# Performance work log

Measured on AMD Instinct MI355X. Metric: run time of the kernel, lower is better.

## Reference

```python
import jax, jax.numpy as jnp
import numpy as np

S, L, T, E, H = 88, 10, 30, 768, 64  # stocks, lookback days, texts/day, embed, hidden


def setup_inputs() -> dict:
    ks = iter(jax.random.split(jax.random.key(0), 40))

    def p(shape, s=0.05):
        return (jax.random.normal(next(ks), shape) * s).astype(jnp.float32)

    inp = {
        'text_inputs': jax.random.normal(next(ks), (S, L, T, E), jnp.float32),
        'time_inputs': jax.random.uniform(next(ks), (S, L, T), jnp.float32),
        # per-stock TimeLSTM params (torch Linear stored as [in,out])
        'Wd_w': p((S, H, H)), 'Wd_b': p((S, H)),
        'Wall_w': p((S, H, 4 * H)), 'Wall_b': p((S, 4 * H)),
        'Uall_w': p((S, E, 4 * H)), 'Uall_b': p((S, 4 * H)),
        # per-stock text attention
        'tW1_w': p((S, H, H)), 'tW1_b': p((S, H)),
        'tW2_w': p((S, H, H)), 'tW2_b': p((S, H)),
        'tV_w': p((S, H, 1)), 'tV_b': p((S, 1)),
        # per-stock day nn.LSTM cell (h0=0 so W_hh contributes nothing; keep its bias)
        'ih_w': p((S, H, 4 * H)), 'ih_b': p((S, 4 * H)), 'hh_b': p((S, 4 * H)),
        # per-stock day attention
        'dW1_w': p((S, H, H)), 'dW1_b': p((S, H)),
        'dW2_w': p((S, H, H)), 'dW2_b': p((S, H)),
        'dV_w': p((S, H, 1)), 'dV_b': p((S, 1)),
        # shared prediction head
        'pred_w': p((H, 1)), 'pred_b': p((1,)),
    }
    return inp


def _fast_forward(text_inputs, time_inputs, Wd_w, Wd_b, Wall_w, Wall_b, Uall_w, Uall_b,
                  tW1_w, tW1_b, tW2_w, tW2_b, tV_w, tV_b,
                  ih_w, ih_b, hh_b, dW1_w, dW1_b, dW2_w, dW2_b, dV_w, dV_b,
                  pred_w, pred_b):
    # Precompute input projection U_all(x): [S,L,T,4H]
    u = jnp.einsum('slte,seg->sltg', text_inputs, Uall_w) + Uall_b[:, None, None, :]

    def step(carry, xs):
        h, c = carry                      # each [S,L,H]
        u_t, ts_t = xs                    # [S,L,4H], [S,L]
        c_s1 = jnp.tanh(jnp.einsum('slh,shk->slk', c, Wd_w) + Wd_b[:, None, :])
        c_adj = c - c_s1 + c_s1 * ts_t[..., None]
        gates = jnp.einsum('slh,shg->slg', h, Wall_w) + Wall_b[:, None, :] + u_t
        f, i, o, g = jnp.split(jax.nn.sigmoid(gates), 4, axis=-1)  # all sigmoid (incl. candidate, as in source)
        c = f * c_adj + i * g
        h = o * jnp.tanh(c)
        return (h, c), h

    z = jnp.zeros((S, L, H), text_inputs.dtype)
    (h_last, _), hs = jax.lax.scan(step, (z, z), (jnp.moveaxis(u, 2, 0), jnp.moveaxis(time_inputs, 2, 0)))
    full = jnp.moveaxis(hs, 0, 2)  # [S,L,T,H]

    # text attention: softmax over texts T
    a1 = jnp.einsum('slh,shk->slk', h_last, tW1_w) + tW1_b[:, None, :]
    a2 = jnp.einsum('slth,shk->sltk', full, tW2_w) + tW2_b[:, None, None, :]
    score = jnp.einsum('slth,sho->slto', jnp.tanh(a1[:, :, None, :] + a2), tV_w) + tV_b[:, None, None, :]
    attn = jax.nn.softmax(score, axis=2)
    day_vec = jnp.sum(attn * full, axis=2)  # [S,L,H]

    # day nn.LSTM: input (1,L,64) seq-first => seq_len=1, batch=L -> single step from zero state
    gates = jnp.einsum('slh,shg->slg', day_vec, ih_w) + ih_b[:, None, :] + hh_b[:, None, :]
    i_g, f_g, g_g, o_g = jnp.split(gates, 4, axis=-1)  # torch gate order i,f,g,o
    c_d = jax.nn.sigmoid(i_g) * jnp.tanh(g_g)
    h_d = jax.nn.sigmoid(o_g) * jnp.tanh(c_d)  # [S,L,H]; output == h_n since seq_len==1

    # day attention: full == last == h_d, softmax over days L
    b1 = jnp.einsum('slh,shk->slk', h_d, dW1_w) + dW1_b[:, None, :]
    b2 = jnp.einsum('slh,shk->slk', h_d, dW2_w) + dW2_b[:, None, :]
    score_d = jnp.einsum('slh,sho->slo', jnp.tanh(b1 + b2), dV_w) + dV_b[:, None, :]
    attn_d = jax.nn.softmax(score_d, axis=1)
    stock_vec = jnp.sum(attn_d * h_d, axis=1)  # [S,H]

    return jax.nn.leaky_relu(stock_vec @ pred_w + pred_b)  # [S,1], slope 0.01


def reference(text_inputs, time_inputs, Wd_w, Wd_b, Wall_w, Wall_b, Uall_w, Uall_b,
              tW1_w, tW1_b, tW2_w, tW2_b, tV_w, tV_b,
              ih_w, ih_b, hh_b, dW1_w, dW1_b, dW2_w, dW2_b, dV_w, dV_b,
              pred_w, pred_b):
    return _fast_forward(text_inputs, time_inputs, Wd_w, Wd_b, Wall_w, Wall_b, Uall_w, Uall_b,
                         tW1_w, tW1_b, tW2_w, tW2_b, tV_w, tV_b,
                         ih_w, ih_b, hh_b, dW1_w, dW1_b, dW2_w, dW2_b, dV_w, dV_b,
                         pred_w, pred_b)
```

## Files before the change

kernel.cpp:

```cpp
#include <hip/hip_runtime.h>
#include <cmath>

#define NS 88
#define NL 10
#define NT 30
#define NE 768
#define NH 64
#define NG 256
#define NM 300

typedef _Float16 half_t;
typedef __attribute__((ext_vector_type(2))) _Float16 half2_t;
typedef __attribute__((ext_vector_type(8))) _Float16 half8;
typedef __attribute__((ext_vector_type(4))) _Float16 half4v;
typedef __attribute__((ext_vector_type(4))) float f32x4;

__device__ inline void gload_lds16(const void* g, void* l) {
  __builtin_amdgcn_global_load_lds(
      (const __attribute__((address_space(1))) unsigned int*)g,
      (__attribute__((address_space(3))) unsigned int*)l, 16, 0, 0);
}

__device__ inline float fsigmoid(float x) {
  return __builtin_amdgcn_rcpf(1.f + __expf(-x));
}
__device__ inline float ftanh(float x) {
  float e = __expf(2.f * x);
  return 1.f - 2.f * __builtin_amdgcn_rcpf(e + 1.f);
}

#if __has_builtin(__builtin_amdgcn_fdot2)
__device__ inline float fdot2(half2_t a, half2_t b, float c) {
  return __builtin_amdgcn_fdot2(a, b, c, false);
}
#else
__device__ inline float fdot2(half2_t a, half2_t b, float c) {
  return fmaf((float)a[1], (float)b[1], fmaf((float)a[0], (float)b[0], c));
}
#endif

__device__ inline half2_t mk_h2(float a, float b) {
  half2_t r; r[0] = (half_t)a; r[1] = (half_t)b; return r;
}

__global__ __launch_bounds__(256) void convB_kernel(
    const float* __restrict__ in, half_t* __restrict__ out)
{
  __shared__ float tile[32][36];
  int b  = blockIdx.x;
  int s  = b / 192;
  int r  = b % 192;
  int kt = r / 8;
  int nt = r % 8;
  int t  = threadIdx.x;

  int kk  = t >> 3;
  int nn4 = (t & 7) * 4;
  float4 v = *(const float4*)(in + ((size_t)s * NE + kt * 32 + kk) * NG + nt * 32 + nn4);
  tile[kk][nn4 + 0] = v.x; tile[kk][nn4 + 1] = v.y;
  tile[kk][nn4 + 2] = v.z; tile[kk][nn4 + 3] = v.w;
  __syncthreads();

  int nn = t >> 3;
  int kq = (t & 7) * 4;
  half4v o;
#pragma unroll
  for (int j = 0; j < 4; ++j) o[j] = (half_t)tile[kq + j][nn];
  *(half4v*)(out + ((size_t)s * NG + nt * 32 + nn) * NE + kt * 32 + kq) = o;
}

__global__ __launch_bounds__(256) void gemm_mfma_kernel(
    const float*  __restrict__ text,
    const half_t* __restrict__ Bf16,
    const float*  __restrict__ bias,
    float* __restrict__ U)
{
  __shared__ uint4 smem4[1536];
  char* smem = (char*)smem4;

  int b   = blockIdx.x;
  int swz = (b & 7) * 110 + (b >> 3);
  int s   = swz / 10;
  int rr_ = swz % 10;
  int m0  = (rr_ >> 1) * 64;
  int n0  = (rr_ & 1) * 128;

  int tid = threadIdx.x;
  int w = tid >> 6, l = tid & 63;
  int wm = w >> 1, wn = w & 1;
  int lr = l & 15, lk = l >> 4;

  const float*  At = text + (size_t)s * NM * NE;
  const half_t* Bb = Bf16 + ((size_t)s * NG + n0) * NE;

  f32x4 acc[2][4];
#pragma unroll
  for (int i = 0; i < 2; ++i)
#pragma unroll
    for (int j = 0; j < 4; ++j) acc[i][j] = (f32x4){0.f, 0.f, 0.f, 0.f};

  for (int step = 0; step < 12; ++step) {
    int k0 = step * 64;
#pragma unroll
    for (int j = 0; j < 4; ++j) {
      int ci  = j * 256 + tid;
      int row = ci >> 3;
      int c   = (ci & 7) ^ (row & 7);
      gload_lds16(Bb + (size_t)row * NE + k0 + c * 8,
                  smem + 8192 + j * 4096 + w * 1024);
    }
#pragma unroll
    for (int j = 0; j < 2; ++j) {
      int idx = j * 256 + tid;
      int row = idx >> 3, c = idx & 7;
      int m   = m0 + row;
      half8 av;
      if (m < NM) {
        const float* p = At + (size_t)m * NE + k0 + c * 8;
        float4 x = *(const float4*)p;
        float4 y = *(const float4*)(p + 4);
        av[0] = (half_t)x.x; av[1] = (half_t)x.y;
        av[2] = (half_t)x.z; av[3] = (half_t)x.w;
        av[4] = (half_t)y.x; av[5] = (half_t)y.y;
        av[6] = (half_t)y.z; av[7] = (half_t)y.w;
      } else {
#pragma unroll
        for (int q = 0; q < 8; ++q) av[q] = (half_t)0.f;
      }
      *(half8*)(smem + row * 128 + ((c ^ (row & 7)) * 16)) = av;
    }
    __syncthreads();

#pragma unroll
    for (int kk = 0; kk < 2; ++kk) {
      half8 af[2], bf[4];
#pragma unroll
      for (int fm = 0; fm < 2; ++fm) {
        int rw = wm * 32 + fm * 16 + lr;
        int cc = (kk * 4 + lk) ^ (rw & 7);
        af[fm] = *(const half8*)(smem + rw * 128 + cc * 16);
      }
#pragma unroll
      for (int fn = 0; fn < 4; ++fn) {
        int rw = wn * 64 + fn * 16 + lr;
        int cc = (kk * 4 + lk) ^ (rw & 7);
        bf[fn] = *(const half8*)(smem + 8192 + rw * 128 + cc * 16);
      }
#pragma unroll
      for (int fm = 0; fm < 2; ++fm)
#pragma unroll
        for (int fn = 0; fn < 4; ++fn)
          acc[fm][fn] = __builtin_amdgcn_mfma_f32_16x16x32_f16(
              af[fm], bf[fn], acc[fm][fn], 0, 0, 0);
    }
    __syncthreads();
  }

#pragma unroll
  for (int fn = 0; fn < 4; ++fn) {
    int col = n0 + wn * 64 + fn * 16 + lr;
    float bv = bias[(size_t)s * NG + col];
#pragma unroll
    for (int fm = 0; fm < 2; ++fm) {
      int mbase = m0 + wm * 32 + fm * 16 + lk * 4;
#pragma unroll
      for (int e = 0; e < 4; ++e) {
        int m = mbase + e;
        if (m < NM)
          U[((size_t)s * NM + m) * NG + col] = acc[fm][fn][e] + bv;
      }
    }
  }
}

__global__ __launch_bounds__(64) void lstm_attn_kernel(
    const float* __restrict__ u,
    const float* __restrict__ time_in,
    const float* __restrict__ Wdw,  const float* __restrict__ Wdb,
    const float* __restrict__ Wallw, const float* __restrict__ Wallb,
    const float* __restrict__ tW1w, const float* __restrict__ tW1b,
    const float* __restrict__ tW2w, const float* __restrict__ tW2b,
    const float* __restrict__ tVw,  const float* __restrict__ tVb,
    float* __restrict__ day_vec)
{
  int bid = blockIdx.x;
  int s = bid / NL;
  int j = threadIdx.x;

  __shared__ float   u_s[NT * NG];
  __shared__ float   hist[NT][NH];
  __shared__ float   ts_s[NT];
  __shared__ half2_t h2_s[NH / 2];
  __shared__ half2_t c2_s[NH / 2];

  const float* u_base = u + (size_t)bid * NT * NG;
#pragma unroll
  for (int i = 0; i < NT; ++i)
    gload_lds16(u_base + i * NG + j * 4, (char*)u_s + i * 1024);

  if (j < NT) ts_s[j] = time_in[(size_t)bid * NT + j];
  ((half_t*)h2_s)[j] = (half_t)0.f;
  ((half_t*)c2_s)[j] = (half_t)0.f;

  const float* Wa  = Wallw + (size_t)s * NH * NG;
  const float* Wdp = Wdw   + (size_t)s * NH * NH;
  half2_t wf[32], wi[32], wo[32], wg[32], wd[32];
#pragma unroll
  for (int k2 = 0; k2 < 32; ++k2) {
    wf[k2] = mk_h2(Wa[(2*k2) * NG + j],        Wa[(2*k2+1) * NG + j]);
    wi[k2] = mk_h2(Wa[(2*k2) * NG + 64 + j],   Wa[(2*k2+1) * NG + 64 + j]);
    wo[k2] = mk_h2(Wa[(2*k2) * NG + 128 + j],  Wa[(2*k2+1) * NG + 128 + j]);
    wg[k2] = mk_h2(Wa[(2*k2) * NG + 192 + j],  Wa[(2*k2+1) * NG + 192 + j]);
    wd[k2] = mk_h2(Wdp[(2*k2) * NH + j],       Wdp[(2*k2+1) * NH + j]);
  }
  float bf = Wallb[(size_t)s * NG + j];
  float bi = Wallb[(size_t)s * NG + 64 + j];
  float bo = Wallb[(size_t)s * NG + 128 + j];
  float bg = Wallb[(size_t)s * NG + 192 + j];
  float bd = Wdb[(size_t)s * NH + j];

  asm volatile("s_waitcnt vmcnt(0)" ::: "memory");

  float c_my = 0.f;
  for (int t = 0; t < NT; ++t) {
    float accf = bf + u_s[t * NG + j];
    float acci = bi + u_s[t * NG + 64 + j];
    float acco = bo + u_s[t * NG + 128 + j];
    float accg = bg + u_s[t * NG + 192 + j];
    float accd = bd;
#pragma unroll
    for (int k2 = 0; k2 < 32; ++k2) {
      half2_t hv = h2_s[k2];
      half2_t cv = c2_s[k2];
      accf = fdot2(hv, wf[k2], accf);
      acci = fdot2(hv, wi[k2], acci);
      acco = fdot2(hv, wo[k2], acco);
      accg = fdot2(hv, wg[k2], accg);
      accd = fdot2(cv, wd[k2], accd);
    }
    float f  = fsigmoid(accf);
    float ii = fsigmoid(acci);
    float o  = fsigmoid(acco);
    float gg = fsigmoid(accg);
    float cadj = c_my + ftanh(accd) * (ts_s[t] - 1.f);
    float cn = fmaf(f, cadj, ii * gg);
    c_my = cn;
    float hn = o * ftanh(cn);
    ((half_t*)h2_s)[j] = (half_t)hn;
    ((half_t*)c2_s)[j] = (half_t)cn;
    hist[t][j] = hn;
  }

  const float* tW1p = tW1w + (size_t)s * NH * NH;
  const float* tW2p = tW2w + (size_t)s * NH * NH;

  float tw2c[NH];
#pragma unroll
  for (int h = 0; h < NH; ++h) tw2c[h] = tW2p[(size_t)h * NH + j];

  float a1 = tW1b[(size_t)s * NH + j];
  {
    const float4* h4 = (const float4*)&hist[NT - 1][0];
#pragma unroll
    for (int q = 0; q < NH / 4; ++q) {
      float4 v = h4[q];
      a1 = fmaf(v.x, tW1p[(size_t)(4*q+0) * NH + j], a1);
      a1 = fmaf(v.y, tW1p[(size_t)(4*q+1) * NH + j], a1);
      a1 = fmaf(v.z, tW1p[(size_t)(4*q+2) * NH + j], a1);
      a1 = fmaf(v.w, tW1p[(size_t)(4*q+3) * NH + j], a1);
    }
  }
  float b2k = tW2b[(size_t)s * NH + j];
  float tv  = tVw[(size_t)s * NH + j];
  float tvb = tVb[s];

  float sc[NT];
#pragma unroll
  for (int t = 0; t < NT; ++t) {
    float a2 = b2k;
    const float4* h4 = (const float4*)&hist[t][0];
#pragma unroll
    for (int q = 0; q < NH / 4; ++q) {
      float4 v = h4[q];
      a2 = fmaf(v.x, tw2c[4*q+0], a2);
      a2 = fmaf(v.y, tw2c[4*q+1], a2);
      a2 = fmaf(v.z, tw2c[4*q+2], a2);
      a2 = fmaf(v.w, tw2c[4*q+3], a2);
    }
    float v = ftanh(a1 + a2) * tv;
#pragma unroll
    for (int off = 32; off >= 1; off >>= 1) v += __shfl_xor(v, off);
    sc[t] = v + tvb;
  }
  float mx = sc[0];
#pragma unroll
  for (int t = 1; t < NT; ++t) mx = fmaxf(mx, sc[t]);
  float sum = 0.f;
#pragma unroll
  for (int t = 0; t < NT; ++t) { sc[t] = __expf(sc[t] - mx); sum += sc[t]; }
  float inv = __builtin_amdgcn_rcpf(sum);
  float dv = 0.f;
#pragma unroll
  for (int t = 0; t < NT; ++t) dv = fmaf(sc[t] * inv, hist[t][j], dv);
  day_vec[(size_t)bid * NH + j] = dv;
}

__global__ __launch_bounds__(256) void day_head_kernel(
    const float* __restrict__ day_vec,
    const float* __restrict__ ihw, const float* __restrict__ ihb,
    const float* __restrict__ hhb,
    const float* __restrict__ dW1w, const float* __restrict__ dW1b,
    const float* __restrict__ dW2w, const float* __restrict__ dW2b,
    const float* __restrict__ dVw,  const float* __restrict__ dVb,
    const float* __restrict__ predw, const float* __restrict__ predb,
    float* __restrict__ out)
{
  int s = blockIdx.x;
  int g = threadIdx.x;
  int j = g & 63;
  int q = g >> 6;

  __shared__ float dv_s[NL][NH];
  __shared__ float gl[NL][NG];
  __shared__ float hd[NL][NH];

  for (int i = g; i < NL * NH; i += 256)
    ((float*)dv_s)[i] = day_vec[(size_t)s * NL * NH + i];
  __syncthreads();

  float ihcol[NH];
#pragma unroll
  for (int k = 0; k < NH; ++k)
    ihcol[k] = ihw[((size_t)s * NH + k) * NG + g];
  float bias = ihb[(size_t)s * NG + g] + hhb[(size_t)s * NG + g];

  bool is_gpart = (g >= 128 && g < 192);
  for (int l = 0; l < NL; ++l) {
    float acc = bias;
#pragma unroll
    for (int k = 0; k < NH; ++k) acc = fmaf(dv_s[l][k], ihcol[k], acc);
    gl[l][g] = is_gpart ? ftanh(acc) : fsigmoid(acc);
  }
  __syncthreads();
  for (int l = q; l < NL; l += 4) {
    float cd = gl[l][j] * gl[l][128 + j];
    hd[l][j] = gl[l][192 + j] * ftanh(cd);
  }
  __syncthreads();

  if (g < 64) {
    int k = g;
    float dw1c[NH], dw2c[NH];
#pragma unroll
    for (int h = 0; h < NH; ++h) {
      dw1c[h] = dW1w[((size_t)s * NH + h) * NH + k];
      dw2c[h] = dW2w[((size_t)s * NH + h) * NH + k];
    }
    float b1 = dW1b[(size_t)s * NH + k];
    float b2 = dW2b[(size_t)s * NH + k];
    float dv = dVw[(size_t)s * NH + k];
    float dvb = dVb[s];

    float sc[NL];
#pragma unroll
    for (int l = 0; l < NL; ++l) {
      float x1 = b1, x2 = b2;
#pragma unroll
      for (int h = 0; h < NH; ++h) {
        x1 = fmaf(hd[l][h], dw1c[h], x1);
        x2 = fmaf(hd[l][h], dw2c[h], x2);
      }
      float v = ftanh(x1 + x2) * dv;
#pragma unroll
      for (int off = 32; off >= 1; off >>= 1) v += __shfl_xor(v, off);
      sc[l] = v + dvb;
    }
    float mx = sc[0];
#pragma unroll
    for (int l = 1; l < NL; ++l) mx = fmaxf(mx, sc[l]);
    float sum = 0.f;
#pragma unroll
    for (int l = 0; l < NL; ++l) { sc[l] = __expf(sc[l] - mx); sum += sc[l]; }
    float inv = __builtin_amdgcn_rcpf(sum);
    float sv = 0.f;
#pragma unroll
    for (int l = 0; l < NL; ++l) sv = fmaf(sc[l] * inv, hd[l][k], sv);

    float p = sv * predw[k];
#pragma unroll
    for (int off = 32; off >= 1; off >>= 1) p += __shfl_xor(p, off);
    if (k == 0) {
      float x = p + predb[0];
      out[s] = (x >= 0.f) ? x : 0.01f * x;
    }
  }
}

extern "C" void kernel_launch(void* const* d_in, const int* in_sizes, int n_in,
                              void* d_out, int out_size, void* d_ws, size_t ws_size,
                              hipStream_t stream) {
  (void)in_sizes; (void)n_in; (void)out_size; (void)ws_size;

  const float* text    = (const float*)d_in[0];
  const float* time_in = (const float*)d_in[1];
  const float* Wdw     = (const float*)d_in[2];
  const float* Wdb     = (const float*)d_in[3];
  const float* Wallw   = (const float*)d_in[4];
  const float* Wallb   = (const float*)d_in[5];
  const float* Uallw   = (const float*)d_in[6];
  const float* Uallb   = (const float*)d_in[7];
  const float* tW1w    = (const float*)d_in[8];
  const float* tW1b    = (const float*)d_in[9];
  const float* tW2w    = (const float*)d_in[10];
  const float* tW2b    = (const float*)d_in[11];
  const float* tVw     = (const float*)d_in[12];
  const float* tVb     = (const float*)d_in[13];
  const float* ihw     = (const float*)d_in[14];
  const float* ihb     = (const float*)d_in[15];
  const float* hhb     = (const float*)d_in[16];
  const float* dW1w    = (const float*)d_in[17];
  const float* dW1b    = (const float*)d_in[18];
  const float* dW2w    = (const float*)d_in[19];
  const float* dW2b    = (const float*)d_in[20];
  const float* dVw     = (const float*)d_in[21];
  const float* dVb     = (const float*)d_in[22];
  const float* predw   = (const float*)d_in[23];
  const float* predb   = (const float*)d_in[24];

  float* ws      = (float*)d_ws;
  float* u       = ws;
  float* day_vec = u + (size_t)NS * NM * NG;
  half_t* Bf16   = (half_t*)(day_vec + (size_t)NS * NL * NH);

  convB_kernel<<<NS * 192, 256, 0, stream>>>(Uallw, Bf16);
  gemm_mfma_kernel<<<NS * 10, 256, 0, stream>>>(text, Bf16, Uallb, u);
  lstm_attn_kernel<<<NS * NL, 64, 0, stream>>>(u, time_in, Wdw, Wdb,
                                               Wallw, Wallb,
                                               tW1w, tW1b, tW2w, tW2b,
                                               tVw, tVb, day_vec);
  day_head_kernel<<<NS, 256, 0, stream>>>(day_vec, ihw, ihb, hhb,
                                          dW1w, dW1b, dW2w, dW2b, dVw, dVb,
                                          predw, predb, (float*)d_out);
}
```

Measured before the change: 104.7 us.

## Enlarge GEMM tile to 128x256 with double-buffered LDS prefetch

The per-stock projection GEMM now uses 512-thread blocks that each compute a 128x256 output tile, covering the full gate width, instead of 64x128 tiles. The LDS A and B buffers are double-buffered, so the next k-slice's global loads are issued before the current slice's MFMAs and one barrier per step is dropped. This cuts redundant A reads across N tiles and hides load latency. The cost is far fewer blocks (264 vs 880), 96KB of LDS per block, and more accumulator registers, which may hurt occupancy and leave CUs idle.

```diff
diff --git a/kernel.cpp b/kernel.cpp
--- a/kernel.cpp
+++ b/kernel.cpp
@@ -69,54 +69,51 @@
   *(half4v*)(out + ((size_t)s * NG + nt * 32 + nn) * NE + kt * 32 + kq) = o;
 }
 
-__global__ __launch_bounds__(256) void gemm_mfma_kernel(
+__global__ __launch_bounds__(512) void gemm_mfma_kernel(
     const float*  __restrict__ text,
     const half_t* __restrict__ Bf16,
     const float*  __restrict__ bias,
     float* __restrict__ U)
 {
-  __shared__ uint4 smem4[1536];
+  __shared__ uint4 smem4[6144];
   char* smem = (char*)smem4;
 
   int b   = blockIdx.x;
-  int swz = (b & 7) * 110 + (b >> 3);
-  int s   = swz / 10;
-  int rr_ = swz % 10;
-  int m0  = (rr_ >> 1) * 64;
-  int n0  = (rr_ & 1) * 128;
+  int swz = (b & 7) * 33 + (b >> 3);
+  int s   = swz / 3;
+  int m0  = (swz % 3) * 128;
 
   int tid = threadIdx.x;
   int w = tid >> 6, l = tid & 63;
-  int wm = w >> 1, wn = w & 1;
+  int wm = w >> 2, wn = w & 3;
   int lr = l & 15, lk = l >> 4;
 
   const float*  At = text + (size_t)s * NM * NE;
-  const half_t* Bb = Bf16 + ((size_t)s * NG + n0) * NE;
-
-  f32x4 acc[2][4];
-#pragma unroll
-  for (int i = 0; i < 2; ++i)
+  const half_t* Bb = Bf16 + (size_t)s * NG * NE;
+
+  f32x4 acc[4][4];
+#pragma unroll
+  for (int i = 0; i < 4; ++i)
 #pragma unroll
     for (int j = 0; j < 4; ++j) acc[i][j] = (f32x4){0.f, 0.f, 0.f, 0.f};
 
-  for (int step = 0; step < 12; ++step) {
-    int k0 = step * 64;
+  {
 #pragma unroll
     for (int j = 0; j < 4; ++j) {
-      int ci  = j * 256 + tid;
+      int ci  = j * 512 + tid;
       int row = ci >> 3;
       int c   = (ci & 7) ^ (row & 7);
-      gload_lds16(Bb + (size_t)row * NE + k0 + c * 8,
-                  smem + 8192 + j * 4096 + w * 1024);
+      gload_lds16(Bb + (size_t)row * NE + c * 8,
+                  smem + 32768 + j * 8192 + w * 1024);
     }
 #pragma unroll
     for (int j = 0; j < 2; ++j) {
-      int idx = j * 256 + tid;
+      int idx = j * 512 + tid;
       int row = idx >> 3, c = idx & 7;
       int m   = m0 + row;
       half8 av;
       if (m < NM) {
-        const float* p = At + (size_t)m * NE + k0 + c * 8;
+        const float* p = At + (size_t)m * NE + c * 8;
         float4 x = *(const float4*)p;
         float4 y = *(const float4*)(p + 4);
         av[0] = (half_t)x.x; av[1] = (half_t)x.y;
@@ -130,39 +127,89 @@
       *(half8*)(smem + row * 128 + ((c ^ (row & 7)) * 16)) = av;
     }
     __syncthreads();
+  }
+
+  for (int step = 0; step < 12; ++step) {
+    int cur = step & 1;
+    char* Ac = smem + cur * 16384;
+    char* Bc = smem + 32768 + cur * 32768;
+    bool has_next = (step < 11);
+    int k1 = (step + 1) * 64;
+
+    float4 ax[2], ay[2];
+    if (has_next) {
+      char* Bn = smem + 32768 + (cur ^ 1) * 32768;
+#pragma unroll
+      for (int j = 0; j < 2; ++j) {
+        int idx = j * 512 + tid;
+        int row = idx >> 3, c = idx & 7;
+        int m   = m0 + row;
+        if (m < NM) {
+          const float* p = At + (size_t)m * NE + k1 + c * 8;
+          ax[j] = *(const float4*)p;
+          ay[j] = *(const float4*)(p + 4);
+        } else {
+          ax[j] = (float4){0.f,0.f,0.f,0.f};
+          ay[j] = (float4){0.f,0.f,0.f,0.f};
+        }
+      }
+#pragma unroll
+      for (int j = 0; j < 4; ++j) {
+        int ci  = j * 512 + tid;
+        int row = ci >> 3;
+        int c   = (ci & 7) ^ (row & 7);
+        gload_lds16(Bb + (size_t)row * NE + k1 + c * 8,
+                    Bn + j * 8192 + w * 1024);
+      }
+    }
 
 #pragma unroll
     for (int kk = 0; kk < 2; ++kk) {
-      half8 af[2], bf[4];
-#pragma unroll
-      for (int fm = 0; fm < 2; ++fm) {
-        int rw = wm * 32 + fm * 16 + lr;
+      half8 af[4], bf[4];
+#pragma unroll
+      for (int fm = 0; fm < 4; ++fm) {
+        int rw = wm * 64 + fm * 16 + lr;
         int cc = (kk * 4 + lk) ^ (rw & 7);
-        af[fm] = *(const half8*)(smem + rw * 128 + cc * 16);
+        af[fm] = *(const half8*)(Ac + rw * 128 + cc * 16);
       }
 #pragma unroll
       for (int fn = 0; fn < 4; ++fn) {
         int rw = wn * 64 + fn * 16 + lr;
         int cc = (kk * 4 + lk) ^ (rw & 7);
-        bf[fn] = *(const half8*)(smem + 8192 + rw * 128 + cc * 16);
-      }
-#pragma unroll
-      for (int fm = 0; fm < 2; ++fm)
+        bf[fn] = *(const half8*)(Bc + rw * 128 + cc * 16);
+      }
+#pragma unroll
+      for (int fm = 0; fm < 4; ++fm)
 #pragma unroll
         for (int fn = 0; fn < 4; ++fn)
           acc[fm][fn] = __builtin_amdgcn_mfma_f32_16x16x32_f16(
               af[fm], bf[fn], acc[fm][fn], 0, 0, 0);
     }
-    __syncthreads();
+
+    if (has_next) {
+      char* An = smem + (cur ^ 1) * 16384;
+#pragma unroll
+      for (int j = 0; j < 2; ++j) {
+        int idx = j * 512 + tid;
+        int row = idx >> 3, c = idx & 7;
+        half8 av;
+        av[0] = (half_t)ax[j].x; av[1] = (half_t)ax[j].y;
+        av[2] = (half_t)ax[j].z; av[3] = (half_t)ax[j].w;
+        av[4] = (half_t)ay[j].x; av[5] = (half_t)ay[j].y;
+        av[6] = (half_t)ay[j].z; av[7] = (half_t)ay[j].w;
+        *(half8*)(An + row * 128 + ((c ^ (row & 7)) * 16)) = av;
+      }
+      __syncthreads();
+    }
   }
 
 #pragma unroll
   for (int fn = 0; fn < 4; ++fn) {
-    int col = n0 + wn * 64 + fn * 16 + lr;
+    int col = wn * 64 + fn * 16 + lr;
     float bv = bias[(size_t)s * NG + col];
 #pragma unroll
-    for (int fm = 0; fm < 2; ++fm) {
-      int mbase = m0 + wm * 32 + fm * 16 + lk * 4;
+    for (int fm = 0; fm < 4; ++fm) {
+      int mbase = m0 + wm * 64 + fm * 16 + lk * 4;
 #pragma unroll
       for (int e = 0; e < 4; ++e) {
         int m = mbase + e;
@@ -433,7 +480,7 @@
   half_t* Bf16   = (half_t*)(day_vec + (size_t)NS * NL * NH);
 
   convB_kernel<<<NS * 192, 256, 0, stream>>>(Uallw, Bf16);
-  gemm_mfma_kernel<<<NS * 10, 256, 0, stream>>>(text, Bf16, Uallb, u);
+  gemm_mfma_kernel<<<NS * 3, 512, 0, stream>>>(text, Bf16, Uallb, u);
   lstm_attn_kernel<<<NS * NL, 64, 0, stream>>>(u, time_in, Wdw, Wdb,
                                                Wallw, Wallb,
                                                tW1w, tW1b, tW2w, tW2b,
```

After: 121.1 us. 1.16x slower.

## Pipeline GEMM with triple-buffered LDS and larger 128x128 tiles

Applied to the files above, without the earlier changes.

Reworks the input-projection GEMM to use 128x128 output tiles (6 blocks per stock instead of 10), a K-step of 32, and a three-stage LDS ring. Global loads of A into registers and async B loads into LDS are issued two stages ahead, with explicit vmcnt waits, so memory latency overlaps the MFMA work. Raw s_barrier calls replace __syncthreads. This doubles LDS use and raises register pressure, cuts the block count to 528 (lower occupancy and wave count), and depends on hand-counted waitcnt values being correct.

```diff
diff --git a/kernel.cpp b/kernel.cpp
--- a/kernel.cpp
+++ b/kernel.cpp
@@ -20,6 +20,9 @@
       (const __attribute__((address_space(1))) unsigned int*)g,
       (__attribute__((address_space(3))) unsigned int*)l, 16, 0, 0);
 }
+
+#define WAITV(N) asm volatile("s_waitcnt vmcnt(" #N ")" ::: "memory")
+#define LGKM0    asm volatile("s_waitcnt lgkmcnt(0)" ::: "memory")
 
 __device__ inline float fsigmoid(float x) {
   return __builtin_amdgcn_rcpf(1.f + __expf(-x));
@@ -75,15 +78,15 @@
     const float*  __restrict__ bias,
     float* __restrict__ U)
 {
-  __shared__ uint4 smem4[1536];
+  __shared__ uint4 smem4[3072];
   char* smem = (char*)smem4;
 
   int b   = blockIdx.x;
-  int swz = (b & 7) * 110 + (b >> 3);
-  int s   = swz / 10;
-  int rr_ = swz % 10;
-  int m0  = (rr_ >> 1) * 64;
-  int n0  = (rr_ & 1) * 128;
+  int swz = (b & 7) * 66 + (b >> 3);
+  int s   = swz / 6;
+  int r   = swz % 6;
+  int m0  = (r >> 1) * 128;
+  int n0  = (r & 1) * 128;
 
   int tid = threadIdx.x;
   int w = tid >> 6, l = tid & 63;
@@ -93,76 +96,119 @@
   const float*  At = text + (size_t)s * NM * NE;
   const half_t* Bb = Bf16 + ((size_t)s * NG + n0) * NE;
 
-  f32x4 acc[2][4];
-#pragma unroll
-  for (int i = 0; i < 2; ++i)
+  f32x4 acc[4][4];
+#pragma unroll
+  for (int i = 0; i < 4; ++i)
 #pragma unroll
     for (int j = 0; j < 4; ++j) acc[i][j] = (f32x4){0.f, 0.f, 0.f, 0.f};
 
-  for (int step = 0; step < 12; ++step) {
-    int k0 = step * 64;
-#pragma unroll
-    for (int j = 0; j < 4; ++j) {
-      int ci  = j * 256 + tid;
-      int row = ci >> 3;
-      int c   = (ci & 7) ^ (row & 7);
-      gload_lds16(Bb + (size_t)row * NE + k0 + c * 8,
-                  smem + 8192 + j * 4096 + w * 1024);
-    }
-#pragma unroll
-    for (int j = 0; j < 2; ++j) {
-      int idx = j * 256 + tid;
-      int row = idx >> 3, c = idx & 7;
-      int m   = m0 + row;
-      half8 av;
-      if (m < NM) {
-        const float* p = At + (size_t)m * NE + k0 + c * 8;
-        float4 x = *(const float4*)p;
-        float4 y = *(const float4*)(p + 4);
-        av[0] = (half_t)x.x; av[1] = (half_t)x.y;
-        av[2] = (half_t)x.z; av[3] = (half_t)x.w;
-        av[4] = (half_t)y.x; av[5] = (half_t)y.y;
-        av[6] = (half_t)y.z; av[7] = (half_t)y.w;
-      } else {
-#pragma unroll
-        for (int q = 0; q < 8; ++q) av[q] = (half_t)0.f;
-      }
-      *(half8*)(smem + row * 128 + ((c ^ (row & 7)) * 16)) = av;
-    }
-    __syncthreads();
-
-#pragma unroll
-    for (int kk = 0; kk < 2; ++kk) {
-      half8 af[2], bf[4];
-#pragma unroll
-      for (int fm = 0; fm < 2; ++fm) {
-        int rw = wm * 32 + fm * 16 + lr;
-        int cc = (kk * 4 + lk) ^ (rw & 7);
-        af[fm] = *(const half8*)(smem + rw * 128 + cc * 16);
-      }
-#pragma unroll
-      for (int fn = 0; fn < 4; ++fn) {
-        int rw = wn * 64 + fn * 16 + lr;
-        int cc = (kk * 4 + lk) ^ (rw & 7);
-        bf[fn] = *(const half8*)(smem + 8192 + rw * 128 + cc * 16);
-      }
-#pragma unroll
-      for (int fm = 0; fm < 2; ++fm)
-#pragma unroll
-        for (int fn = 0; fn < 4; ++fn)
-          acc[fm][fn] = __builtin_amdgcn_mfma_f32_16x16x32_f16(
-              af[fm], bf[fn], acc[fm][fn], 0, 0, 0);
-    }
-    __syncthreads();
-  }
+  float4 ra0[2][2], ra1[2][2];
+
+#define STAGE_ISSUE(K, RA)                                                   \
+  {                                                                          \
+    int kOff = (K) * 32;                                                     \
+    _Pragma("unroll")                                                        \
+    for (int j = 0; j < 2; ++j) {                                            \
+      int idx = j * 256 + tid;                                               \
+      int row = idx >> 2;                                                    \
+      int m   = m0 + row;                                                    \
+      const float* p = At + (size_t)(m < NM ? m : NM - 1) * NE + kOff +      \
+                       (idx & 3) * 8;                                        \
+      RA[j][0] = *(const float4*)p;                                          \
+      RA[j][1] = *(const float4*)(p + 4);                                    \
+    }                                                                        \
+    char* Bdst = smem + ((K) % 3) * 16384 + 8192;                            \
+    _Pragma("unroll")                                                        \
+    for (int j = 0; j < 2; ++j) {                                            \
+      int ci  = j * 256 + tid;                                               \
+      int row = ci >> 2;                                                     \
+      int c   = (ci & 3) ^ (row & 3);                                        \
+      gload_lds16(Bb + (size_t)row * NE + (K) * 32 + c * 8,                  \
+                  Bdst + j * 4096 + w * 1024);                               \
+    }                                                                        \
+  }
+
+#define STAGE_WRITE_A(K, RA)                                                 \
+  {                                                                          \
+    char* Adst = smem + ((K) % 3) * 16384;                                   \
+    _Pragma("unroll")                                                        \
+    for (int j = 0; j < 2; ++j) {                                            \
+      int idx = j * 256 + tid;                                               \
+      int row = idx >> 2, c = idx & 3;                                       \
+      int m   = m0 + row;                                                    \
+      half8 av;                                                              \
+      av[0] = (half_t)RA[j][0].x; av[1] = (half_t)RA[j][0].y;                \
+      av[2] = (half_t)RA[j][0].z; av[3] = (half_t)RA[j][0].w;                \
+      av[4] = (half_t)RA[j][1].x; av[5] = (half_t)RA[j][1].y;                \
+      av[6] = (half_t)RA[j][1].z; av[7] = (half_t)RA[j][1].w;                \
+      if (m >= NM) {                                                         \
+        _Pragma("unroll")                                                    \
+        for (int q = 0; q < 8; ++q) av[q] = (half_t)0.f;                     \
+      }                                                                      \
+      *(half8*)(Adst + row * 64 + ((c ^ (row & 3)) * 16)) = av;              \
+    }                                                                        \
+  }
+
+#define COMPUTE(K)                                                           \
+  {                                                                          \
+    char* Abuf = smem + ((K) % 3) * 16384;                                   \
+    char* Bbuf = Abuf + 8192;                                                \
+    half8 af[4], bf[4];                                                      \
+    _Pragma("unroll")                                                        \
+    for (int fm = 0; fm < 4; ++fm) {                                         \
+      int rw = wm * 64 + fm * 16 + lr;                                       \
+      af[fm] = *(const half8*)(Abuf + rw * 64 + ((lk ^ (rw & 3)) * 16));     \
+    }                                                                        \
+    _Pragma("unroll")                                                        \
+    for (int fn = 0; fn < 4; ++fn) {                                         \
+      int rw = wn * 64 + fn * 16 + lr;                                       \
+      bf[fn] = *(const half8*)(Bbuf + rw * 64 + ((lk ^ (rw & 3)) * 16));     \
+    }                                                                        \
+    _Pragma("unroll")                                                        \
+    for (int fm = 0; fm < 4; ++fm)                                           \
+      _Pragma("unroll")                                                      \
+      for (int fn = 0; fn < 4; ++fn)                                         \
+        acc[fm][fn] = __builtin_amdgcn_mfma_f32_16x16x32_f16(                \
+            af[fm], bf[fn], acc[fm][fn], 0, 0, 0);                           \
+  }
+
+  STAGE_ISSUE(0, ra0);
+  STAGE_ISSUE(1, ra1);
+  WAITV(8);
+  STAGE_WRITE_A(0, ra0);
+  LGKM0;
+  __builtin_amdgcn_s_barrier();
+
+#pragma unroll 1
+  for (int kb = 0; kb < 24; kb += 2) {
+    if (kb + 2 < 24) STAGE_ISSUE(kb + 2, ra0);
+    if (kb + 2 < 24) { WAITV(6); } else { WAITV(0); }
+    if (kb + 1 < 24) STAGE_WRITE_A(kb + 1, ra1);
+    COMPUTE(kb);
+    LGKM0;
+    __builtin_amdgcn_s_barrier();
+
+    int k1 = kb + 1;
+    if (k1 + 2 < 24) STAGE_ISSUE(k1 + 2, ra1);
+    if (k1 + 2 < 24) { WAITV(6); } else { WAITV(0); }
+    if (k1 + 1 < 24) STAGE_WRITE_A(k1 + 1, ra0);
+    COMPUTE(k1);
+    if (k1 < 23) {
+      LGKM0;
+      __builtin_amdgcn_s_barrier();
+    }
+  }
+#undef STAGE_ISSUE
+#undef STAGE_WRITE_A
+#undef COMPUTE
 
 #pragma unroll
   for (int fn = 0; fn < 4; ++fn) {
     int col = n0 + wn * 64 + fn * 16 + lr;
     float bv = bias[(size_t)s * NG + col];
 #pragma unroll
-    for (int fm = 0; fm < 2; ++fm) {
-      int mbase = m0 + wm * 32 + fm * 16 + lk * 4;
+    for (int fm = 0; fm < 4; ++fm) {
+      int mbase = m0 + wm * 64 + fm * 16 + lk * 4;
 #pragma unroll
       for (int e = 0; e < 4; ++e) {
         int m = mbase + e;
@@ -433,7 +479,7 @@
   half_t* Bf16   = (half_t*)(day_vec + (size_t)NS * NL * NH);
 
   convB_kernel<<<NS * 192, 256, 0, stream>>>(Uallw, Bf16);
-  gemm_mfma_kernel<<<NS * 10, 256, 0, stream>>>(text, Bf16, Uallb, u);
+  gemm_mfma_kernel<<<NS * 6, 256, 0, stream>>>(text, Bf16, Uallb, u);
   lstm_attn_kernel<<<NS * NL, 64, 0, stream>>>(u, time_in, Wdw, Wdb,
                                                Wallw, Wallb,
                                                tW1w, tW1b, tW2w, tW2b,
```

After: 132.9 us. +26.9%, slower.

## Split GEMM K dimension in two and sum partials in LSTM kernel

Applied to the files above, without the earlier changes.

The U projection GEMM is split along K into two halves, doubling the block count from 880 to 1760 so more CUs are busy, and each half writes its own partial buffer with bias added only in the first. The LSTM kernel drops the LDS prefetch of u and instead reads both partials directly from global memory each timestep, summing them into the gate pre-activations. This trades better GEMM occupancy for twice the U write and read traffic, plus per-step global loads on the latency-bound recurrence path in place of the upfront async LDS load.

```diff
diff --git a/kernel.cpp b/kernel.cpp
--- a/kernel.cpp
+++ b/kernel.cpp
@@ -8,6 +8,7 @@
 #define NH 64
 #define NG 256
 #define NM 300
+#define NKS 2
 
 typedef _Float16 half_t;
 typedef __attribute__((ext_vector_type(2))) _Float16 half2_t;
@@ -73,17 +74,20 @@
     const float*  __restrict__ text,
     const half_t* __restrict__ Bf16,
     const float*  __restrict__ bias,
-    float* __restrict__ U)
+    float* __restrict__ Upart)
 {
   __shared__ uint4 smem4[1536];
   char* smem = (char*)smem4;
 
   int b   = blockIdx.x;
-  int swz = (b & 7) * 110 + (b >> 3);
-  int s   = swz / 10;
-  int rr_ = swz % 10;
-  int m0  = (rr_ >> 1) * 64;
-  int n0  = (rr_ & 1) * 128;
+  int swz = (b & 7) * 220 + (b >> 3);
+  int s    = swz / 20;
+  int rem  = swz % 20;
+  int ks   = rem / 10;
+  int rr_  = rem % 10;
+  int m0   = (rr_ >> 1) * 64;
+  int n0   = (rr_ & 1) * 128;
+  int kbase = ks * (NE / NKS);
 
   int tid = threadIdx.x;
   int w = tid >> 6, l = tid & 63;
@@ -99,8 +103,8 @@
 #pragma unroll
     for (int j = 0; j < 4; ++j) acc[i][j] = (f32x4){0.f, 0.f, 0.f, 0.f};
 
-  for (int step = 0; step < 12; ++step) {
-    int k0 = step * 64;
+  for (int step = 0; step < (NE / NKS) / 64; ++step) {
+    int k0 = kbase + step * 64;
 #pragma unroll
     for (int j = 0; j < 4; ++j) {
       int ci  = j * 256 + tid;
@@ -156,10 +160,11 @@
     __syncthreads();
   }
 
+  float* U = Upart + (size_t)ks * ((size_t)NS * NM * NG);
 #pragma unroll
   for (int fn = 0; fn < 4; ++fn) {
     int col = n0 + wn * 64 + fn * 16 + lr;
-    float bv = bias[(size_t)s * NG + col];
+    float bv = (ks == 0) ? bias[(size_t)s * NG + col] : 0.f;
 #pragma unroll
     for (int fm = 0; fm < 2; ++fm) {
       int mbase = m0 + wm * 32 + fm * 16 + lk * 4;
@@ -187,16 +192,14 @@
   int s = bid / NL;
   int j = threadIdx.x;
 
-  __shared__ float   u_s[NT * NG];
   __shared__ float   hist[NT][NH];
   __shared__ float   ts_s[NT];
   __shared__ half2_t h2_s[NH / 2];
   __shared__ half2_t c2_s[NH / 2];
 
-  const float* u_base = u + (size_t)bid * NT * NG;
-#pragma unroll
-  for (int i = 0; i < NT; ++i)
-    gload_lds16(u_base + i * NG + j * 4, (char*)u_s + i * 1024);
+  const size_t UP = (size_t)NS * NM * NG;
+  const float* up0 = u + (size_t)bid * NT * NG;
+  const float* up1 = up0 + UP;
 
   if (j < NT) ts_s[j] = time_in[(size_t)bid * NT + j];
   ((half_t*)h2_s)[j] = (half_t)0.f;
@@ -219,33 +222,33 @@
   float bg = Wallb[(size_t)s * NG + 192 + j];
   float bd = Wdb[(size_t)s * NH + j];
 
-  asm volatile("s_waitcnt vmcnt(0)" ::: "memory");
-
   float c_my = 0.f;
   for (int t = 0; t < NT; ++t) {
-    float accf = bf + u_s[t * NG + j];
-    float acci = bi + u_s[t * NG + 64 + j];
-    float acco = bo + u_s[t * NG + 128 + j];
-    float accg = bg + u_s[t * NG + 192 + j];
-    float accd = bd;
+    int o = t * NG + j;
+    float u0f = up0[o],       u1f = up1[o];
+    float u0i = up0[o + 64],  u1i = up1[o + 64];
+    float u0o = up0[o + 128], u1o = up1[o + 128];
+    float u0g = up0[o + 192], u1g = up1[o + 192];
+
+    float dotf = 0.f, doti = 0.f, doto = 0.f, dotg = 0.f, dotd = 0.f;
 #pragma unroll
     for (int k2 = 0; k2 < 32; ++k2) {
       half2_t hv = h2_s[k2];
       half2_t cv = c2_s[k2];
-      accf = fdot2(hv, wf[k2], accf);
-      acci = fdot2(hv, wi[k2], acci);
-      acco = fdot2(hv, wo[k2], acco);
-      accg = fdot2(hv, wg[k2], accg);
-      accd = fdot2(cv, wd[k2], accd);
-    }
-    float f  = fsigmoid(accf);
-    float ii = fsigmoid(acci);
-    float o  = fsigmoid(acco);
-    float gg = fsigmoid(accg);
-    float cadj = c_my + ftanh(accd) * (ts_s[t] - 1.f);
+      dotf = fdot2(hv, wf[k2], dotf);
+      doti = fdot2(hv, wi[k2], doti);
+      doto = fdot2(hv, wo[k2], doto);
+      dotg = fdot2(hv, wg[k2], dotg);
+      dotd = fdot2(cv, wd[k2], dotd);
+    }
+    float f  = fsigmoid(dotf + bf + u0f + u1f);
+    float ii = fsigmoid(doti + bi + u0i + u1i);
+    float o_ = fsigmoid(doto + bo + u0o + u1o);
+    float gg = fsigmoid(dotg + bg + u0g + u1g);
+    float cadj = c_my + ftanh(dotd + bd) * (ts_s[t] - 1.f);
     float cn = fmaf(f, cadj, ii * gg);
     c_my = cn;
-    float hn = o * ftanh(cn);
+    float hn = o_ * ftanh(cn);
     ((half_t*)h2_s)[j] = (half_t)hn;
     ((half_t*)c2_s)[j] = (half_t)cn;
     hist[t][j] = hn;
@@ -428,13 +431,13 @@
   const float* predb   = (const float*)d_in[24];
 
   float* ws      = (float*)d_ws;
-  float* u       = ws;
-  float* day_vec = u + (size_t)NS * NM * NG;
+  float* u_part  = ws;
+  float* day_vec = u_part + (size_t)NKS * NS * NM * NG;
   half_t* Bf16   = (half_t*)(day_vec + (size_t)NS * NL * NH);
 
   convB_kernel<<<NS * 192, 256, 0, stream>>>(Uallw, Bf16);
-  gemm_mfma_kernel<<<NS * 10, 256, 0, stream>>>(text, Bf16, Uallb, u);
-  lstm_attn_kernel<<<NS * NL, 64, 0, stream>>>(u, time_in, Wdw, Wdb,
+  gemm_mfma_kernel<<<NS * 10 * NKS, 256, 0, stream>>>(text, Bf16, Uallb, u_part);
+  lstm_attn_kernel<<<NS * NL, 64, 0, stream>>>(u_part, time_in, Wdw, Wdb,
                                                Wallw, Wallb,
                                                tW1w, tW1b, tW2w, tW2b,
                                                tVw, tVb, day_vec);
```

Result: slower. 131.7 us (+25.8%).
